# Kernel optimization log

Hardware: AMD Instinct MI355X
Metric: run time of the kernel (lower is better)

Reference implementation:

```python
import jax, jax.numpy as jnp
import numpy as np

BN_EPS = 1e-5

def batch_norm(x, gamma, beta):
    # training-mode BatchNorm1d: biased batch stats over the edge dim
    mean = jnp.mean(x, axis=0)
    var = jnp.var(x, axis=0)
    return (x - mean) * jax.lax.rsqrt(var + BN_EPS) * gamma + beta

def setup_inputs() -> dict:
    key = jax.random.key(0)
    ks = jax.random.split(key, 10)
    N, F, E = 50000, 128, 600000
    D_in = 2 * F + 12  # 268
    h = jax.random.normal(ks[0], (N, F), dtype=jnp.float32)
    edge_feature = jax.random.normal(ks[1], (E, 12), dtype=jnp.float32)
    src = jax.random.randint(ks[2], (E,), 0, N)
    dst = jax.random.randint(ks[3], (E,), 0, N)
    def lin(k, fan_in, shape):
        bound = 1.0 / np.sqrt(fan_in)
        return jax.random.uniform(k, shape, jnp.float32, -bound, bound)
    W1 = lin(ks[4], D_in, (28, D_in)); b1 = lin(ks[5], D_in, (28,))
    W2 = lin(ks[6], 28, (8, 28));      b2 = lin(ks[7], 28, (8,))
    W3 = lin(ks[8], 8, (1, 8));        b3 = lin(ks[9], 8, (1,))
    gamma1 = jnp.ones((28,), jnp.float32); beta1 = jnp.zeros((28,), jnp.float32)
    gamma2 = jnp.ones((8,), jnp.float32);  beta2 = jnp.zeros((8,), jnp.float32)
    return {"h": h, "edge_feature": edge_feature, "src": src, "dst": dst,
            "W1": W1, "b1": b1, "gamma1": gamma1, "beta1": beta1,
            "W2": W2, "b2": b2, "gamma2": gamma2, "beta2": beta2,
            "W3": W3, "b3": b3}

def reference(h, edge_feature, src, dst, W1, b1, gamma1, beta1,
              W2, b2, gamma2, beta2, W3, b3):
    h_u = h[src]                    # [E, F] gather of source node feats
    h_v = h[dst]                    # [E, F] gather of dest node feats
    x = jnp.concatenate([h_u, h_v, edge_feature], axis=1)  # [E, 2F+12]
    s = jax.nn.relu(batch_norm(x @ W1.T + b1, gamma1, beta1))  # [E, 28]
    s = jax.nn.relu(batch_norm(s @ W2.T + b2, gamma2, beta2))  # [E, 8]
    score = s @ W3.T + b3           # [E, 1]
    return score
```

## Files before the change

### kernel.cpp

```cpp
#include <hip/hip_runtime.h>

#define BN_EPS 1e-5f


__global__ void k1_proj(const float* __restrict__ h, const float* __restrict__ W1,
                        float* __restrict__ Psrc, float* __restrict__ Pdst,
                        float* __restrict__ stats, int N) {
  if (blockIdx.x == 0 && threadIdx.x < 72) stats[threadIdx.x] = 0.f;
  const int half = blockIdx.x & 1;
  const int node = (blockIdx.x >> 1) * 256 + threadIdx.x;
  if (node >= N) return;

  const float* __restrict__ wbase = W1 + half * 128;
  const float4* __restrict__ h4 = (const float4*)(h + (size_t)node * 128);

  float acc[28];
#pragma unroll
  for (int c = 0; c < 28; c++) acc[c] = 0.f;

  for (int kk = 0; kk < 16; kk++) {
    const float4 a = h4[kk * 2];
    const float4 b = h4[kk * 2 + 1];
#pragma unroll
    for (int c = 0; c < 28; c++) {
      const float* w = wbase + c * 268 + kk * 8;
      acc[c] += a.x * w[0] + a.y * w[1] + a.z * w[2] + a.w * w[3]
              + b.x * w[4] + b.y * w[5] + b.z * w[6] + b.w * w[7];
    }
  }

  float4* po = (float4*)((half ? Pdst : Psrc) + (size_t)node * 32);
#pragma unroll
  for (int q = 0; q < 7; q++) {
    po[q] = make_float4(acc[q * 4], acc[q * 4 + 1], acc[q * 4 + 2], acc[q * 4 + 3]);
  }
  po[7] = make_float4(0.f, 0.f, 0.f, 0.f);
}

__global__ void k2_edge(const float* __restrict__ Psrc, const float* __restrict__ Pdst,
                        const float* __restrict__ ef,
                        const int* __restrict__ src, const int* __restrict__ dst,
                        const float* __restrict__ W1, const float* __restrict__ b1,
                        float* __restrict__ y1, float* __restrict__ stats, int E) {
  const int tid = threadIdx.x;
  const int c = tid & 31;
  const int g = tid >> 5;
  const bool act = (c < 28);
  float w[12];
  float bias = 0.f;
  if (act) {
    const float4* wp = (const float4*)(W1 + c * 268 + 256);
    float4 w0 = wp[0], w1 = wp[1], w2 = wp[2];
    w[0] = w0.x; w[1] = w0.y; w[2] = w0.z; w[3] = w0.w;
    w[4] = w1.x; w[5] = w1.y; w[6] = w1.z; w[7] = w1.w;
    w[8] = w2.x; w[9] = w2.y; w[10] = w2.z; w[11] = w2.w;
    bias = b1[c];
  }
  float sum = 0.f, ssq = 0.f;
  const int gstride = gridDim.x * 8;
  for (int e = blockIdx.x * 8 + g; e < E; e += gstride) {
    const int s = src[e], d = dst[e];
    if (act) {
      const float pa = Psrc[(size_t)s * 32 + c];
      const float pb = Pdst[(size_t)d * 32 + c];
      const float4* e4 = (const float4*)(ef + (size_t)e * 12);
      float4 f0 = e4[0], f1 = e4[1], f2 = e4[2];
      float acc = bias
          + f0.x * w[0] + f0.y * w[1] + f0.z * w[2] + f0.w * w[3]
          + f1.x * w[4] + f1.y * w[5] + f1.z * w[6] + f1.w * w[7]
          + f2.x * w[8] + f2.y * w[9] + f2.z * w[10] + f2.w * w[11];
      const float v = acc + pa + pb;
      y1[(size_t)e * 28 + c] = v;
      sum += v;
      ssq += v * v;
    }
  }
  sum += __shfl_xor(sum, 32);
  ssq += __shfl_xor(ssq, 32);
  __shared__ float red[2][4][28];
  const int wave = tid >> 6, lane = tid & 63;
  if (lane < 28) { red[0][wave][lane] = sum; red[1][wave][lane] = ssq; }
  __syncthreads();
  if (tid < 28) {
    atomicAdd(&stats[tid], red[0][0][tid] + red[0][1][tid] + red[0][2][tid] + red[0][3][tid]);
    atomicAdd(&stats[28 + tid], red[1][0][tid] + red[1][1][tid] + red[1][2][tid] + red[1][3][tid]);
  }
}

__global__ void k3_fin1(const float* __restrict__ gamma, const float* __restrict__ beta,
                        float* __restrict__ stats, float invE) {
  const int c = threadIdx.x;
  if (c < 28) {
    const float mean = stats[c] * invE;
    const float var = stats[28 + c] * invE - mean * mean;
    const float sc = gamma[c] * rsqrtf(var + BN_EPS);
    stats[72 + c] = sc;
    stats[100 + c] = beta[c] - mean * sc;
  }
}

__global__ void k4_l2(const float* __restrict__ y1, const float* __restrict__ statsRO,
                      const float* __restrict__ W2, const float* __restrict__ b2,
                      float* __restrict__ y2, float* __restrict__ statsW, int E) {
  __shared__ float tile[256 * 29];
  float as[8], aq[8];
#pragma unroll
  for (int o = 0; o < 8; o++) { as[o] = 0.f; aq[o] = 0.f; }

  for (int tileBase = blockIdx.x * 256; tileBase < E; tileBase += gridDim.x * 256) {
    const int nEdge = min(256, E - tileBase);
    const int total = nEdge * 28;
    const float* gp = y1 + (size_t)tileBase * 28;
    for (int j = threadIdx.x * 4; j < total; j += 1024) {
      const float4 v = *(const float4*)(gp + j);
      const int e = j / 28;
      const int cc = j - e * 28;
      float* lr = &tile[e * 29 + cc];
      lr[0] = v.x; lr[1] = v.y; lr[2] = v.z; lr[3] = v.w;
    }
    __syncthreads();
    if ((int)threadIdx.x < nEdge) {
      const float* s1 = &tile[threadIdx.x * 29];
      float acc[8];
#pragma unroll
      for (int o = 0; o < 8; o++) acc[o] = b2[o];
#pragma unroll
      for (int cc = 0; cc < 28; cc++) {
        const float s = fmaxf(s1[cc] * statsRO[72 + cc] + statsRO[100 + cc], 0.f);
#pragma unroll
        for (int o = 0; o < 8; o++) acc[o] += W2[o * 28 + cc] * s;
      }
      float4* yo = (float4*)(y2 + (size_t)(tileBase + threadIdx.x) * 8);
      yo[0] = make_float4(acc[0], acc[1], acc[2], acc[3]);
      yo[1] = make_float4(acc[4], acc[5], acc[6], acc[7]);
#pragma unroll
      for (int o = 0; o < 8; o++) { as[o] += acc[o]; aq[o] += acc[o] * acc[o]; }
    }
    __syncthreads();
  }

#pragma unroll
  for (int o = 0; o < 8; o++) {
    for (int off = 32; off; off >>= 1) {
      as[o] += __shfl_down(as[o], off);
      aq[o] += __shfl_down(aq[o], off);
    }
  }
  __shared__ float redS[4][16];
  const int wave = threadIdx.x >> 6, lane = threadIdx.x & 63;
  if (lane == 0) {
#pragma unroll
    for (int o = 0; o < 8; o++) { redS[wave][o] = as[o]; redS[wave][8 + o] = aq[o]; }
  }
  __syncthreads();
  if (threadIdx.x < 16) {
    const int t = threadIdx.x;
    atomicAdd(&statsW[56 + t], redS[0][t] + redS[1][t] + redS[2][t] + redS[3][t]);
  }
}

__global__ void k5_fin2(const float* __restrict__ gamma, const float* __restrict__ beta,
                        float* __restrict__ stats, float invE) {
  const int c = threadIdx.x;
  if (c < 8) {
    const float mean = stats[56 + c] * invE;
    const float var = stats[64 + c] * invE - mean * mean;
    const float sc = gamma[c] * rsqrtf(var + BN_EPS);
    stats[128 + c] = sc;
    stats[136 + c] = beta[c] - mean * sc;
  }
}

__global__ void k6_l3(const float* __restrict__ y2, const float* __restrict__ stats,
                      const float* __restrict__ W3, const float* __restrict__ b3,
                      float* __restrict__ out, int E) {
  const int e = blockIdx.x * blockDim.x + threadIdx.x;
  if (e >= E) return;
  const float4* p = (const float4*)(y2 + (size_t)e * 8);
  float4 a = p[0], b4 = p[1];
  float v[8] = {a.x, a.y, a.z, a.w, b4.x, b4.y, b4.z, b4.w};
  float acc = b3[0];
#pragma unroll
  for (int o = 0; o < 8; o++) {
    float s = fmaxf(v[o] * stats[128 + o] + stats[136 + o], 0.f);
    acc += W3[o] * s;
  }
  out[e] = acc;
}

extern "C" void kernel_launch(void* const* d_in, const int* in_sizes, int n_in,
                              void* d_out, int out_size, void* d_ws, size_t ws_size,
                              hipStream_t stream) {
  const float* h   = (const float*)d_in[0];
  const float* ef  = (const float*)d_in[1];
  const int* src   = (const int*)d_in[2];
  const int* dst   = (const int*)d_in[3];
  const float* W1  = (const float*)d_in[4];
  const float* b1  = (const float*)d_in[5];
  const float* g1  = (const float*)d_in[6];
  const float* be1 = (const float*)d_in[7];
  const float* W2  = (const float*)d_in[8];
  const float* b2  = (const float*)d_in[9];
  const float* g2  = (const float*)d_in[10];
  const float* be2 = (const float*)d_in[11];
  const float* W3  = (const float*)d_in[12];
  const float* b3  = (const float*)d_in[13];
  float* out = (float*)d_out;

  const int N = in_sizes[0] / 128;
  const int E = in_sizes[2];
  const float invE = 1.0f / (float)E;

  float* ws = (float*)d_ws;
  float* stats = ws;
  float* Psrc = ws + 256;
  float* y1 = Psrc + (size_t)N * 32;
  float* y2 = y1 + (size_t)E * 28;
  float* Pdst = y2;

  const int nodeBlocks = (N + 255) / 256;
  const int nTiles = (E + 255) / 256;
  k1_proj<<<nodeBlocks * 2, 256, 0, stream>>>(h, W1, Psrc, Pdst, stats, N);
  k2_edge<<<1280, 256, 0, stream>>>(Psrc, Pdst, ef, src, dst, W1, b1, y1, stats, E);
  k3_fin1<<<1, 32, 0, stream>>>(g1, be1, stats, invE);
  k4_l2<<<nTiles, 256, 0, stream>>>(y1, stats, W2, b2, y2, stats, E);
  k5_fin2<<<1, 64, 0, stream>>>(g2, be2, stats, invE);
  k6_l3<<<nTiles, 256, 0, stream>>>(y2, stats, W3, b3, out, E);
}
```

Baseline: 298.4 us.

## Software-pipeline edge gather in k2 with 4-deep register prefetch and per-group edge chunks

Each 32-lane group in k2_edge now handles a contiguous chunk of 32 edges instead of a grid-strided loop. The src and dst indices for the chunk are loaded once and broadcast with shuffles. A four-stage rotating register pipeline issues the Psrc, Pdst and edge-feature loads for edges up to four ahead of the compute, to hide gather latency. The grid grows to one block per 256 edges, which raises the block count and the number of stats atomics, and adds register pressure from the prefetch buffers.

After: 317.3 us. 1.06x slower.

```diff
diff --git a/kernel.cpp b/kernel.cpp
--- a/kernel.cpp
+++ b/kernel.cpp
@@ -36,6 +36,28 @@
   }
   po[7] = make_float4(0.f, 0.f, 0.f, 0.f);
 }
+
+#define K2_REFILL(S, J)                                                     \
+  if ((J) < 32) {                                                           \
+    s##S = __shfl(sAll, (J), 32); d##S = __shfl(dAll, (J), 32);             \
+    pa##S = Psrc[(size_t)s##S * 32 + c];                                    \
+    pb##S = Pdst[(size_t)d##S * 32 + c];                                    \
+    const float4* e4_ = (const float4*)(ef + (size_t)(base + (J)) * 12);    \
+    f0##S = e4_[0]; f1##S = e4_[1]; f2##S = e4_[2];                         \
+  }
+
+#define K2_COMPUTE(S, EIDX)                                                 \
+  {                                                                         \
+    const float v = bias                                                    \
+      + f0##S.x * w[0] + f0##S.y * w[1] + f0##S.z * w[2] + f0##S.w * w[3]   \
+      + f1##S.x * w[4] + f1##S.y * w[5] + f1##S.z * w[6] + f1##S.w * w[7]   \
+      + f2##S.x * w[8] + f2##S.y * w[9] + f2##S.z * w[10] + f2##S.w * w[11] \
+      + pa##S + pb##S;                                                      \
+    if (act) {                                                              \
+      y1[(size_t)(EIDX) * 28 + c] = v;                                      \
+      sum += v; ssq += v * v;                                               \
+    }                                                                       \
+  }
 
 __global__ void k2_edge(const float* __restrict__ Psrc, const float* __restrict__ Pdst,
                         const float* __restrict__ ef,
@@ -47,6 +69,8 @@
   const int g = tid >> 5;
   const bool act = (c < 28);
   float w[12];
+#pragma unroll
+  for (int k = 0; k < 12; k++) w[k] = 0.f;
   float bias = 0.f;
   if (act) {
     const float4* wp = (const float4*)(W1 + c * 268 + 256);
@@ -57,24 +81,47 @@
     bias = b1[c];
   }
   float sum = 0.f, ssq = 0.f;
-  const int gstride = gridDim.x * 8;
-  for (int e = blockIdx.x * 8 + g; e < E; e += gstride) {
-    const int s = src[e], d = dst[e];
-    if (act) {
-      const float pa = Psrc[(size_t)s * 32 + c];
-      const float pb = Pdst[(size_t)d * 32 + c];
-      const float4* e4 = (const float4*)(ef + (size_t)e * 12);
-      float4 f0 = e4[0], f1 = e4[1], f2 = e4[2];
-      float acc = bias
-          + f0.x * w[0] + f0.y * w[1] + f0.z * w[2] + f0.w * w[3]
-          + f1.x * w[4] + f1.y * w[5] + f1.z * w[6] + f1.w * w[7]
-          + f2.x * w[8] + f2.y * w[9] + f2.z * w[10] + f2.w * w[11];
-      const float v = acc + pa + pb;
-      y1[(size_t)e * 28 + c] = v;
-      sum += v;
-      ssq += v * v;
-    }
-  }
+
+  const int base = blockIdx.x * 256 + g * 32;
+
+  if (base + 32 <= E) {
+    const int sAll = src[base + c];
+    const int dAll = dst[base + c];
+    int sA, dA, sB, dB, sC, dC, sD, dD;
+    float paA, pbA, paB, pbB, paC, pbC, paD, pbD;
+    float4 f0A, f1A, f2A, f0B, f1B, f2B, f0C, f1C, f2C, f0D, f1D, f2D;
+    K2_REFILL(A, 0)
+    K2_REFILL(B, 1)
+    K2_REFILL(C, 2)
+    K2_REFILL(D, 3)
+    for (int i = 0; i < 32; i += 4) {
+      K2_COMPUTE(A, base + i)     K2_REFILL(A, i + 4)
+      K2_COMPUTE(B, base + i + 1) K2_REFILL(B, i + 5)
+      K2_COMPUTE(C, base + i + 2) K2_REFILL(C, i + 6)
+      K2_COMPUTE(D, base + i + 3) K2_REFILL(D, i + 7)
+    }
+  } else if (base < E) {
+    const int nLoc = E - base;
+    for (int i = 0; i < nLoc; i++) {
+      const int e = base + i;
+      const int s = src[e], d = dst[e];
+      if (act) {
+        const float pa = Psrc[(size_t)s * 32 + c];
+        const float pb = Pdst[(size_t)d * 32 + c];
+        const float4* e4 = (const float4*)(ef + (size_t)e * 12);
+        const float4 f0 = e4[0], f1 = e4[1], f2 = e4[2];
+        const float v = bias
+            + f0.x * w[0] + f0.y * w[1] + f0.z * w[2] + f0.w * w[3]
+            + f1.x * w[4] + f1.y * w[5] + f1.z * w[6] + f1.w * w[7]
+            + f2.x * w[8] + f2.y * w[9] + f2.z * w[10] + f2.w * w[11]
+            + pa + pb;
+        y1[(size_t)e * 28 + c] = v;
+        sum += v;
+        ssq += v * v;
+      }
+    }
+  }
+
   sum += __shfl_xor(sum, 32);
   ssq += __shfl_xor(ssq, 32);
   __shared__ float red[2][4][28];
@@ -221,7 +268,7 @@
   const int nodeBlocks = (N + 255) / 256;
   const int nTiles = (E + 255) / 256;
   k1_proj<<<nodeBlocks * 2, 256, 0, stream>>>(h, W1, Psrc, Pdst, stats, N);
-  k2_edge<<<1280, 256, 0, stream>>>(Psrc, Pdst, ef, src, dst, W1, b1, y1, stats, E);
+  k2_edge<<<nTiles, 256, 0, stream>>>(Psrc, Pdst, ef, src, dst, W1, b1, y1, stats, E);
   k3_fin1<<<1, 32, 0, stream>>>(g1, be1, stats, invE);
   k4_l2<<<nTiles, 256, 0, stream>>>(y1, stats, W2, b2, y2, stats, E);
   k5_fin2<<<1, 64, 0, stream>>>(g2, be2, stats, invE);
```

## Remap edge kernel to one thread per edge with vectorized gathers

Applied to the files above, without the earlier changes.

The edge kernel now assigns a whole edge to each thread instead of one channel per lane. Each thread loads the 28-wide projected source and destination rows and the edge features as float4 vectors, reads the edge weights from shared memory, and writes the 28 outputs as float4 stores. Per-channel sums are kept in registers and reduced across the wave with shuffles at the end. This drops the 4 idle lanes per 32 and turns scalar gathers into vector loads, but it raises register pressure (launch bounds set) and makes each thread's stores strided, so coalescing is worse.

Result: slower. 576.0 us (+93.0%).

```diff
diff --git a/kernel.cpp b/kernel.cpp
--- a/kernel.cpp
+++ b/kernel.cpp
@@ -37,53 +37,87 @@
   po[7] = make_float4(0.f, 0.f, 0.f, 0.f);
 }
 
-__global__ void k2_edge(const float* __restrict__ Psrc, const float* __restrict__ Pdst,
-                        const float* __restrict__ ef,
-                        const int* __restrict__ src, const int* __restrict__ dst,
-                        const float* __restrict__ W1, const float* __restrict__ b1,
-                        float* __restrict__ y1, float* __restrict__ stats, int E) {
-  const int tid = threadIdx.x;
-  const int c = tid & 31;
-  const int g = tid >> 5;
-  const bool act = (c < 28);
-  float w[12];
-  float bias = 0.f;
-  if (act) {
-    const float4* wp = (const float4*)(W1 + c * 268 + 256);
-    float4 w0 = wp[0], w1 = wp[1], w2 = wp[2];
-    w[0] = w0.x; w[1] = w0.y; w[2] = w0.z; w[3] = w0.w;
-    w[4] = w1.x; w[5] = w1.y; w[6] = w1.z; w[7] = w1.w;
-    w[8] = w2.x; w[9] = w2.y; w[10] = w2.z; w[11] = w2.w;
-    bias = b1[c];
-  }
-  float sum = 0.f, ssq = 0.f;
-  const int gstride = gridDim.x * 8;
-  for (int e = blockIdx.x * 8 + g; e < E; e += gstride) {
+__global__ __launch_bounds__(256, 3)
+void k2_edge(const float* __restrict__ Psrc, const float* __restrict__ Pdst,
+             const float* __restrict__ ef,
+             const int* __restrict__ src, const int* __restrict__ dst,
+             const float* __restrict__ W1, const float* __restrict__ b1,
+             float* __restrict__ y1, float* __restrict__ stats, int E) {
+  __shared__ float lw[28][12];
+  __shared__ float lb[28];
+  for (int i = threadIdx.x; i < 336; i += 256) {
+    lw[i / 12][i % 12] = W1[(i / 12) * 268 + 256 + (i % 12)];
+  }
+  if (threadIdx.x < 28) lb[threadIdx.x] = b1[threadIdx.x];
+  __syncthreads();
+
+  float sumL[28], ssqL[28];
+#pragma unroll
+  for (int c = 0; c < 28; c++) { sumL[c] = 0.f; ssqL[c] = 0.f; }
+
+  const int stride = gridDim.x * 256;
+  for (int e = blockIdx.x * 256 + threadIdx.x; e < E; e += stride) {
     const int s = src[e], d = dst[e];
-    if (act) {
-      const float pa = Psrc[(size_t)s * 32 + c];
-      const float pb = Pdst[(size_t)d * 32 + c];
-      const float4* e4 = (const float4*)(ef + (size_t)e * 12);
-      float4 f0 = e4[0], f1 = e4[1], f2 = e4[2];
-      float acc = bias
-          + f0.x * w[0] + f0.y * w[1] + f0.z * w[2] + f0.w * w[3]
-          + f1.x * w[4] + f1.y * w[5] + f1.z * w[6] + f1.w * w[7]
-          + f2.x * w[8] + f2.y * w[9] + f2.z * w[10] + f2.w * w[11];
-      const float v = acc + pa + pb;
-      y1[(size_t)e * 28 + c] = v;
-      sum += v;
-      ssq += v * v;
-    }
-  }
-  sum += __shfl_xor(sum, 32);
-  ssq += __shfl_xor(ssq, 32);
-  __shared__ float red[2][4][28];
-  const int wave = tid >> 6, lane = tid & 63;
-  if (lane < 28) { red[0][wave][lane] = sum; red[1][wave][lane] = ssq; }
+    const float4* pa4 = (const float4*)(Psrc + (size_t)s * 32);
+    const float4* pb4 = (const float4*)(Pdst + (size_t)d * 32);
+    const float4* e4 = (const float4*)(ef + (size_t)e * 12);
+
+    float pa[28], pb[28], f[12];
+#pragma unroll
+    for (int q = 0; q < 7; q++) {
+      const float4 t = pa4[q];
+      pa[q * 4] = t.x; pa[q * 4 + 1] = t.y; pa[q * 4 + 2] = t.z; pa[q * 4 + 3] = t.w;
+    }
+#pragma unroll
+    for (int q = 0; q < 7; q++) {
+      const float4 t = pb4[q];
+      pb[q * 4] = t.x; pb[q * 4 + 1] = t.y; pb[q * 4 + 2] = t.z; pb[q * 4 + 3] = t.w;
+    }
+#pragma unroll
+    for (int q = 0; q < 3; q++) {
+      const float4 t = e4[q];
+      f[q * 4] = t.x; f[q * 4 + 1] = t.y; f[q * 4 + 2] = t.z; f[q * 4 + 3] = t.w;
+    }
+
+    float v[28];
+#pragma unroll
+    for (int c = 0; c < 28; c++) {
+      const float4* lw4 = (const float4*)(&lw[c][0]);
+      const float4 w0 = lw4[0], w1 = lw4[1], w2 = lw4[2];
+      float acc = lb[c]
+          + f[0] * w0.x + f[1] * w0.y + f[2] * w0.z + f[3] * w0.w
+          + f[4] * w1.x + f[5] * w1.y + f[6] * w1.z + f[7] * w1.w
+          + f[8] * w2.x + f[9] * w2.y + f[10] * w2.z + f[11] * w2.w;
+      acc += pa[c] + pb[c];
+      v[c] = acc;
+      sumL[c] += acc;
+      ssqL[c] += acc * acc;
+    }
+
+    float4* yo = (float4*)(y1 + (size_t)e * 28);
+#pragma unroll
+    for (int q = 0; q < 7; q++) {
+      yo[q] = make_float4(v[q * 4], v[q * 4 + 1], v[q * 4 + 2], v[q * 4 + 3]);
+    }
+  }
+
+  __shared__ float redS[4][28];
+  __shared__ float redQ[4][28];
+  const int wave = threadIdx.x >> 6, lane = threadIdx.x & 63;
+#pragma unroll
+  for (int c = 0; c < 28; c++) {
+    float s = sumL[c], q = ssqL[c];
+    for (int off = 32; off; off >>= 1) {
+      s += __shfl_xor(s, off);
+      q += __shfl_xor(q, off);
+    }
+    if (lane == 0) { redS[wave][c] = s; redQ[wave][c] = q; }
+  }
   __syncthreads();
-  if (tid < 28) {
-    atomicAdd(&stats[tid], red[0][0][tid] + red[0][1][tid] + red[0][2][tid] + red[0][3][tid]);
-    atomicAdd(&stats[28 + tid], red[1][0][tid] + red[1][1][tid] + red[1][2][tid] + red[1][3][tid]);
+  if (threadIdx.x < 28) {
+    const int c = threadIdx.x;
+    atomicAdd(&stats[c], redS[0][c] + redS[1][c] + redS[2][c] + redS[3][c]);
+    atomicAdd(&stats[28 + c], redQ[0][c] + redQ[1][c] + redQ[2][c] + redQ[3][c]);
   }
 }
 
@@ -221,7 +255,7 @@
   const int nodeBlocks = (N + 255) / 256;
   const int nTiles = (E + 255) / 256;
   k1_proj<<<nodeBlocks * 2, 256, 0, stream>>>(h, W1, Psrc, Pdst, stats, N);
-  k2_edge<<<1280, 256, 0, stream>>>(Psrc, Pdst, ef, src, dst, W1, b1, y1, stats, E);
+  k2_edge<<<1172, 256, 0, stream>>>(Psrc, Pdst, ef, src, dst, W1, b1, y1, stats, E);
   k3_fin1<<<1, 32, 0, stream>>>(g1, be1, stats, invE);
   k4_l2<<<nTiles, 256, 0, stream>>>(y1, stats, W2, b2, y2, stats, E);
   k5_fin2<<<1, 64, 0, stream>>>(g2, be2, stats, invE);
```
